# Kernel optimization log

Hardware: AMD Instinct MI355X
Metric: run time of the kernel (lower is better)

## Reference

```python
import jax, jax.numpy as jnp
import numpy as np

ALPHA = 1.0
BETA = 10.0
MARGIN = 0.5


def setup_inputs() -> dict:
    key = jax.random.key(0)
    k1, k2 = jax.random.split(key)
    emb = jax.random.normal(k1, (4096, 512), dtype=jnp.float32)
    # module docstring: embeddings are L2-normalized
    emb = emb / jnp.linalg.norm(emb, axis=1, keepdims=True)
    labels = jax.random.randint(k2, (4096,), 0, 64, dtype=jnp.int64)
    return {"embeddings": emb, "labels": labels}


def reference(embeddings, labels):
    n = embeddings.shape[0]
    sim = embeddings @ embeddings.T  # [n, n]
    labels_eq = labels[None, :] == labels[:, None]
    eye = jnp.eye(n, dtype=bool)
    pos_mask = labels_eq & ~eye
    neg_mask = ~labels_eq & ~eye

    # masked exp-sums (masked entries contribute 0, matching torch's
    # clone/NEG_INF/zero-out dance without materializing extra copies)
    pos_exp = jnp.where(pos_mask, jnp.exp(-ALPHA * (sim - MARGIN)), 0.0)
    neg_exp = jnp.where(neg_mask, jnp.exp(BETA * (sim - MARGIN)), 0.0)
    pos_term = (1.0 / ALPHA) * jnp.log1p(pos_exp.sum(axis=1))
    neg_term = (1.0 / BETA) * jnp.log1p(neg_exp.sum(axis=1))

    valid = pos_mask.any(axis=1) & neg_mask.any(axis=1)
    n_valid = valid.sum()
    total = jnp.where(valid, pos_term + neg_term, 0.0).sum()
    return jnp.where(n_valid > 0, total / jnp.maximum(n_valid, 1).astype(sim.dtype), 0.0)
```

## Files before the change

kernel.cpp:

```cpp
#include <hip/hip_runtime.h>
#include <hip/hip_bf16.h>

#define N 4096
#define D 512
#define MARGIN 0.5f
#define BETA 10.0f

typedef __attribute__((ext_vector_type(8))) short short8;
typedef __attribute__((ext_vector_type(4))) float floatx4;

__device__ inline unsigned short f2bf(float f) {
    unsigned u = __float_as_uint(f);
    u += 0x7fffu + ((u >> 16) & 1u);
    return (unsigned short)(u >> 16);
}

#define GLOAD_LDS16(gp, lp)                                             \
    __builtin_amdgcn_global_load_lds(                                   \
        (const __attribute__((address_space(1))) void*)(gp),            \
        (__attribute__((address_space(3))) void*)(lp), 16, 0, 0)

__global__ __launch_bounds__(256) void convert_bf16_kernel(
        const float4* __restrict__ in, ushort4* __restrict__ out,
        float* __restrict__ sums ) {
    int idx = blockIdx.x * 256 + threadIdx.x;
    if (idx < 2 * N) sums[idx] = 0.f;
    float4 v = in[idx];
    ushort4 o;
    o.x = f2bf(v.x); o.y = f2bf(v.y); o.z = f2bf(v.z); o.w = f2bf(v.w);
    out[idx] = o;
}

__global__ __launch_bounds__(256, 2) void ms_loss_gemm(
        const unsigned short* __restrict__ Ebf,
        const int* __restrict__ labels,
        float* __restrict__ pos_sum,
        float* __restrict__ neg_sum) {
    __shared__ char Als[2][128 * 128];
    __shared__ char Bls[2][128 * 128];
    __shared__ int rlab[128];
    __shared__ int clab[128];

    int t = blockIdx.x;
    int bi = 0;
    while (t >= (32 - bi)) { t -= (32 - bi); ++bi; }
    const int bj = bi + t;
    const bool diag = (bi == bj);

    const int tid  = threadIdx.x;
    const int wave = tid >> 6;
    const int lane = tid & 63;
    const int quad = lane >> 4;
    const int lcol = lane & 15;
    const int wrow = wave >> 1;
    const int wcol = wave & 1;
    const int ibase = bi * 128;
    const int jbase = bj * 128;

    if (tid < 128)       rlab[tid]       = labels[ibase + tid];
    else                 clab[tid - 128] = labels[jbase + tid - 128];

    floatx4 acc[4][4];
#pragma unroll
    for (int mt = 0; mt < 4; ++mt)
#pragma unroll
        for (int nt = 0; nt < 4; ++nt)
            acc[mt][nt] = (floatx4){0.f, 0.f, 0.f, 0.f};

    const char* Eb = (const char*)Ebf;
    const int srow = lane >> 3;
    const int sck  = ((lane & 7) ^ (lane >> 3)) * 16;
    const size_t arow0 = (size_t)(ibase + wave * 8 + srow) * 1024 + sck;
    const size_t brow0 = (size_t)(jbase + wave * 8 + srow) * 1024 + sck;
    const int ldso0 = wave * 1024 + lane * 16;

    const int rsw = (lcol & 7);

#define STAGE(sel, kt_)                                                    \
    {                                                                      \
        const int kb_ = (kt_) * 128;                                       \
        _Pragma("unroll")                                                  \
        for (int it = 0; it < 4; ++it) {                                   \
            GLOAD_LDS16(Eb + arow0 + (size_t)it * 32 * 1024 + kb_,         \
                        Als[sel] + ldso0 + it * 4096);                     \
            if (!diag)                                                     \
                GLOAD_LDS16(Eb + brow0 + (size_t)it * 32 * 1024 + kb_,     \
                            Bls[sel] + ldso0 + it * 4096);                 \
        }                                                                  \
    }

    STAGE(0, 0);

#pragma unroll
    for (int kt = 0; kt < D / 64; ++kt) {
        const int cur = kt & 1;
        __syncthreads();
        if (kt < D / 64 - 1) STAGE(cur ^ 1, kt + 1);

        const char* Ac = Als[cur];
        const char* Bc = diag ? Als[cur] : Bls[cur];
#pragma unroll
        for (int s = 0; s < 2; ++s) {
            short8 a[4], b[4];
            const int rchunk = ((s * 4 + quad) ^ rsw) * 16;
#pragma unroll
            for (int mt = 0; mt < 4; ++mt) {
                int r = wrow * 64 + mt * 16 + lcol;
                a[mt] = *(const short8*)(Ac + r * 128 + rchunk);
            }
#pragma unroll
            for (int nt = 0; nt < 4; ++nt) {
                int c = wcol * 64 + nt * 16 + lcol;
                b[nt] = *(const short8*)(Bc + c * 128 + rchunk);
            }
#pragma unroll
            for (int mt = 0; mt < 4; ++mt)
#pragma unroll
                for (int nt = 0; nt < 4; ++nt)
                    acc[mt][nt] = __builtin_amdgcn_mfma_f32_16x16x32_bf16(
                        a[mt], b[nt], acc[mt][nt], 0, 0, 0);
        }
    }

    int ljv[4], gjv[4];
#pragma unroll
    for (int nt = 0; nt < 4; ++nt) {
        int cl = wcol * 64 + nt * 16 + lcol;
        ljv[nt] = clab[cl];
        gjv[nt] = jbase + cl;
    }

    float colp[4] = {0.f, 0.f, 0.f, 0.f};
    float coln[4] = {0.f, 0.f, 0.f, 0.f};

#pragma unroll
    for (int mt = 0; mt < 4; ++mt) {
#pragma unroll
        for (int reg = 0; reg < 4; ++reg) {
            int rl = wrow * 64 + mt * 16 + quad * 4 + reg;
            int gi = ibase + rl;
            int li = rlab[rl];
            float p = 0.f, ng = 0.f;
#pragma unroll
            for (int nt = 0; nt < 4; ++nt) {
                float s = acc[mt][nt][reg];
                if (gi != gjv[nt]) {
                    if (li == ljv[nt]) {
                        float e = __expf(MARGIN - s);
                        p += e;  colp[nt] += e;
                    } else {
                        float e = __expf(BETA * (s - MARGIN));
                        ng += e; coln[nt] += e;
                    }
                }
            }
            p  += __shfl_xor(p, 1);   ng += __shfl_xor(ng, 1);
            p  += __shfl_xor(p, 2);   ng += __shfl_xor(ng, 2);
            p  += __shfl_xor(p, 4);   ng += __shfl_xor(ng, 4);
            p  += __shfl_xor(p, 8);   ng += __shfl_xor(ng, 8);
            if (lcol == 0) {
                atomicAdd(&pos_sum[gi], p);
                atomicAdd(&neg_sum[gi], ng);
            }
        }
    }

    if (!diag) {
#pragma unroll
        for (int nt = 0; nt < 4; ++nt) {
            float cp = colp[nt], cn = coln[nt];
            cp += __shfl_xor(cp, 16);  cn += __shfl_xor(cn, 16);
            cp += __shfl_xor(cp, 32);  cn += __shfl_xor(cn, 32);
            if (quad == 0) {
                int gj = gjv[nt];
                atomicAdd(&pos_sum[gj], cp);
                atomicAdd(&neg_sum[gj], cn);
            }
        }
    }
}

__global__ __launch_bounds__(256) void finalize_kernel(
        const float4* __restrict__ pos4, const float4* __restrict__ neg4,
        float* __restrict__ out) {
    __shared__ float sb[256];
    __shared__ int   sc[256];
    const int tid = threadIdx.x;
    float tot = 0.f;
    int cnt = 0;
#pragma unroll
    for (int it = 0; it < N / 4 / 256; ++it) {
        int i = it * 256 + tid;
        float4 p = pos4[i];
        float4 ng = neg4[i];
        const float* pp = (const float*)&p;
        const float* nn = (const float*)&ng;
#pragma unroll
        for (int j = 0; j < 4; ++j) {
            if (pp[j] > 0.f && nn[j] > 0.f) {
                tot += log1pf(pp[j]) + (1.0f / BETA) * log1pf(nn[j]);
                cnt += 1;
            }
        }
    }
    sb[tid] = tot; sc[tid] = cnt;
    __syncthreads();
    for (int s = 128; s > 0; s >>= 1) {
        if (tid < s) { sb[tid] += sb[tid + s]; sc[tid] += sc[tid + s]; }
        __syncthreads();
    }
    if (tid == 0) out[0] = (sc[0] > 0) ? sb[0] / (float)sc[0] : 0.f;
}

extern "C" void kernel_launch(void* const* d_in, const int* in_sizes, int n_in,
                              void* d_out, int out_size, void* d_ws, size_t ws_size,
                              hipStream_t stream) {
    const float* emb   = (const float*)d_in[0];
    const int* labels  = (const int*)d_in[1];
    float* out         = (float*)d_out;

    char* ws = (char*)d_ws;
    unsigned short* Ebf = (unsigned short*)ws;
    float* pos_sum = (float*)(ws + (size_t)N * D * 2);
    float* neg_sum = pos_sum + N;

    convert_bf16_kernel<<<(N * D / 4) / 256, 256, 0, stream>>>(
        (const float4*)emb, (ushort4*)Ebf, pos_sum);

    ms_loss_gemm<<<(32 * 33) / 2, 256, 0, stream>>>(Ebf, labels, pos_sum, neg_sum);

    finalize_kernel<<<1, 256, 0, stream>>>(
        (const float4*)pos_sum, (const float4*)neg_sum, out);
}
```

Baseline: 99.37 us.

## Shrink GEMM tiles to 64x64 with single-buffered 128-wide K stages

Changes the symmetric-tile GEMM from 128x128 output tiles (528 blocks) to 64x64 tiles (2080 blocks). Each K stage now covers 128 elements with a single LDS buffer and two barriers per stage, replacing the previous double-buffered 64-wide stages. Launch bounds rise to 4 blocks per SM. The aim is better load balance and occupancy across the 256 CUs. The cost is lower data reuse per tile, more global and L2 traffic, more atomics, and the loss of load/compute overlap.

```diff
diff --git a/kernel.cpp b/kernel.cpp
--- a/kernel.cpp
+++ b/kernel.cpp
@@ -31,19 +31,19 @@
     out[idx] = o;
 }
 
-__global__ __launch_bounds__(256, 2) void ms_loss_gemm(
+__global__ __launch_bounds__(256, 4) void ms_loss_gemm(
         const unsigned short* __restrict__ Ebf,
         const int* __restrict__ labels,
         float* __restrict__ pos_sum,
         float* __restrict__ neg_sum) {
-    __shared__ char Als[2][128 * 128];
-    __shared__ char Bls[2][128 * 128];
-    __shared__ int rlab[128];
-    __shared__ int clab[128];
+    __shared__ char Als[64 * 256];
+    __shared__ char Bls[64 * 256];
+    __shared__ int rlab[64];
+    __shared__ int clab[64];
 
     int t = blockIdx.x;
     int bi = 0;
-    while (t >= (32 - bi)) { t -= (32 - bi); ++bi; }
+    while (t >= (64 - bi)) { t -= (64 - bi); ++bi; }
     const int bj = bi + t;
     const bool diag = (bi == bj);
 
@@ -54,95 +54,92 @@
     const int lcol = lane & 15;
     const int wrow = wave >> 1;
     const int wcol = wave & 1;
-    const int ibase = bi * 128;
-    const int jbase = bj * 128;
-
-    if (tid < 128)       rlab[tid]       = labels[ibase + tid];
-    else                 clab[tid - 128] = labels[jbase + tid - 128];
-
-    floatx4 acc[4][4];
-#pragma unroll
-    for (int mt = 0; mt < 4; ++mt)
-#pragma unroll
-        for (int nt = 0; nt < 4; ++nt)
+    const int ibase = bi * 64;
+    const int jbase = bj * 64;
+
+    if (tid < 64)        rlab[tid]      = labels[ibase + tid];
+    else if (tid < 128)  clab[tid - 64] = labels[jbase + tid - 64];
+
+    floatx4 acc[2][2];
+#pragma unroll
+    for (int mt = 0; mt < 2; ++mt)
+#pragma unroll
+        for (int nt = 0; nt < 2; ++nt)
             acc[mt][nt] = (floatx4){0.f, 0.f, 0.f, 0.f};
 
     const char* Eb = (const char*)Ebf;
-    const int srow = lane >> 3;
-    const int sck  = ((lane & 7) ^ (lane >> 3)) * 16;
-    const size_t arow0 = (size_t)(ibase + wave * 8 + srow) * 1024 + sck;
-    const size_t brow0 = (size_t)(jbase + wave * 8 + srow) * 1024 + sck;
-    const int ldso0 = wave * 1024 + lane * 16;
-
-    const int rsw = (lcol & 7);
-
-#define STAGE(sel, kt_)                                                    \
+    const int srow = lane >> 4;
+    const int sgrp = wave * 4 + srow;
+    const int sck  = ((lane & 15) ^ sgrp) * 16;
+    const size_t aoff0 = (size_t)(ibase + sgrp) * 1024 + sck;
+    const size_t boff0 = (size_t)(jbase + sgrp) * 1024 + sck;
+    const int ldso = wave * 1024 + lane * 16;
+
+#define STAGE(kt_)                                                         \
     {                                                                      \
-        const int kb_ = (kt_) * 128;                                       \
+        const int kb_ = (kt_) * 256;                                       \
         _Pragma("unroll")                                                  \
         for (int it = 0; it < 4; ++it) {                                   \
-            GLOAD_LDS16(Eb + arow0 + (size_t)it * 32 * 1024 + kb_,         \
-                        Als[sel] + ldso0 + it * 4096);                     \
+            GLOAD_LDS16(Eb + aoff0 + (size_t)it * 16384 + kb_,             \
+                        Als + ldso + it * 4096);                           \
             if (!diag)                                                     \
-                GLOAD_LDS16(Eb + brow0 + (size_t)it * 32 * 1024 + kb_,     \
-                            Bls[sel] + ldso0 + it * 4096);                 \
+                GLOAD_LDS16(Eb + boff0 + (size_t)it * 16384 + kb_,         \
+                            Bls + ldso + it * 4096);                       \
         }                                                                  \
     }
 
-    STAGE(0, 0);
-
-#pragma unroll
-    for (int kt = 0; kt < D / 64; ++kt) {
-        const int cur = kt & 1;
+#pragma unroll
+    for (int kt = 0; kt < D / 128; ++kt) {
         __syncthreads();
-        if (kt < D / 64 - 1) STAGE(cur ^ 1, kt + 1);
-
-        const char* Ac = Als[cur];
-        const char* Bc = diag ? Als[cur] : Bls[cur];
-#pragma unroll
-        for (int s = 0; s < 2; ++s) {
-            short8 a[4], b[4];
-            const int rchunk = ((s * 4 + quad) ^ rsw) * 16;
-#pragma unroll
-            for (int mt = 0; mt < 4; ++mt) {
-                int r = wrow * 64 + mt * 16 + lcol;
-                a[mt] = *(const short8*)(Ac + r * 128 + rchunk);
-            }
-#pragma unroll
-            for (int nt = 0; nt < 4; ++nt) {
-                int c = wcol * 64 + nt * 16 + lcol;
-                b[nt] = *(const short8*)(Bc + c * 128 + rchunk);
-            }
-#pragma unroll
-            for (int mt = 0; mt < 4; ++mt)
-#pragma unroll
-                for (int nt = 0; nt < 4; ++nt)
+        STAGE(kt);
+        __syncthreads();
+
+        const char* Ac = Als;
+        const char* Bc = diag ? Als : Bls;
+#pragma unroll
+        for (int s = 0; s < 4; ++s) {
+            short8 a[2], b[2];
+            const int rslot = ((s * 4 + quad) ^ lcol) * 16;
+#pragma unroll
+            for (int mt = 0; mt < 2; ++mt) {
+                int r = wrow * 32 + mt * 16 + lcol;
+                a[mt] = *(const short8*)(Ac + r * 256 + rslot);
+            }
+#pragma unroll
+            for (int nt = 0; nt < 2; ++nt) {
+                int c = wcol * 32 + nt * 16 + lcol;
+                b[nt] = *(const short8*)(Bc + c * 256 + rslot);
+            }
+#pragma unroll
+            for (int mt = 0; mt < 2; ++mt)
+#pragma unroll
+                for (int nt = 0; nt < 2; ++nt)
                     acc[mt][nt] = __builtin_amdgcn_mfma_f32_16x16x32_bf16(
                         a[mt], b[nt], acc[mt][nt], 0, 0, 0);
         }
     }
 
-    int ljv[4], gjv[4];
-#pragma unroll
-    for (int nt = 0; nt < 4; ++nt) {
-        int cl = wcol * 64 + nt * 16 + lcol;
+    int ljv[2], gjv[2];
+#pragma unroll
+    for (int nt = 0; nt < 2; ++nt) {
+        int cl = wcol * 32 + nt * 16 + lcol;
         ljv[nt] = clab[cl];
         gjv[nt] = jbase + cl;
     }
 
-    float colp[4] = {0.f, 0.f, 0.f, 0.f};
-    float coln[4] = {0.f, 0.f, 0.f, 0.f};
-
-#pragma unroll
-    for (int mt = 0; mt < 4; ++mt) {
+    float colp[2] = {0.f, 0.f};
+    float coln[2] = {0.f, 0.f};
+
+#pragma unroll
+    for (int mt = 0; mt < 2; ++mt) {
 #pragma unroll
         for (int reg = 0; reg < 4; ++reg) {
-            int rl = wrow * 64 + mt * 16 + quad * 4 + reg;
+            int rl = wrow * 32 + mt * 16 + quad * 4 + reg;
             int gi = ibase + rl;
             int li = rlab[rl];
             float p = 0.f, ng = 0.f;
 #pragma unroll
-            for (int nt = 0; nt < 4; ++nt) {
+            for (int nt = 0; nt < 2; ++nt) {
                 float s = acc[mt][nt][reg];
                 if (gi != gjv[nt]) {
                     if (li == ljv[nt]) {
@@ -167,7 +164,7 @@
 
     if (!diag) {
 #pragma unroll
-        for (int nt = 0; nt < 4; ++nt) {
+        for (int nt = 0; nt < 2; ++nt) {
             float cp = colp[nt], cn = coln[nt];
             cp += __shfl_xor(cp, 16);  cn += __shfl_xor(cn, 16);
             cp += __shfl_xor(cp, 32);  cn += __shfl_xor(cn, 32);
@@ -227,7 +224,7 @@
     convert_bf16_kernel<<<(N * D / 4) / 256, 256, 0, stream>>>(
         (const float4*)emb, (ushort4*)Ebf, pos_sum);
 
-    ms_loss_gemm<<<(32 * 33) / 2, 256, 0, stream>>>(Ebf, labels, pos_sum, neg_sum);
+    ms_loss_gemm<<<(64 * 65) / 2, 256, 0, stream>>>(Ebf, labels, pos_sum, neg_sum);
 
     finalize_kernel<<<1, 256, 0, stream>>>(
         (const float4*)pos_sum, (const float4*)neg_sum, out);
```

New measurement: 104.9 us. +5.6%, slower.
